# Kernel tuning notes

Measured on AMD Instinct MI355X. Metric: run time of the kernel, lower is better.

## Reference

```python
import jax, jax.numpy as jnp
import numpy as np

B, H, S, D, R = 2, 32, 1024, 128, 16
NB = 4  # max blocks: pre-image, image, pre-assistant-end, post-assistant


def _make_block_mask():
    # Synthetic but realistic block boundaries per sample (derived from the
    # image-token run and assistant-token subsequence positions that the torch
    # module extracts host-side from input_ids).
    bounds = [
        [(0, 16), (16, 272), (272, 603), (603, S)],
        [(0, 8), (8, 264), (264, 501), (501, S)],
    ]
    m = np.zeros((B, NB, S), np.float32)
    for b, blocks in enumerate(bounds):
        for n, (s, e) in enumerate(blocks):
            m[b, n, s:e] = 1.0
    return jnp.asarray(m)


def setup_inputs() -> dict:
    key = jax.random.key(0)
    ks = jax.random.split(key, 7)
    hid = H * D  # 4096
    lo = H * R   # 512
    causal_masked = ~jnp.tril(jnp.ones((S, S), bool))  # True = masked
    return {
        "query_states": jax.random.normal(ks[0], (B, H, S, D), jnp.float32),
        "key_states": jax.random.normal(ks[1], (B, H, S, D), jnp.float32),
        "Wqa": jax.random.normal(ks[2], (lo, hid), jnp.float32) / np.sqrt(hid),
        "Wqb": jax.random.normal(ks[3], (hid, lo), jnp.float32) / np.sqrt(lo),
        "Wka": jax.random.normal(ks[4], (lo, hid), jnp.float32) / np.sqrt(hid),
        "Wkb": jax.random.normal(ks[5], (hid, lo), jnp.float32) / np.sqrt(lo),
        "alpha": jax.random.normal(ks[6], (1,), jnp.float32) * 0.01,  # alpha_std
        "block_mask": _make_block_mask(),  # [B, NB, K] 1.0 inside block
        "attention_mask": jnp.broadcast_to(causal_masked, (B, 1, S, S)),
    }


def reference(query_states, key_states, Wqa, Wqb, Wka, Wkb, alpha, block_mask, attention_mask):
    Bb, Hh, Q, Dd = query_states.shape
    scaling = Dd ** -0.5

    # low-rank Q projection: [B,H,Q,D] -> [B,Q,H*D] -> rank -> back
    q = query_states.transpose(0, 2, 1, 3).reshape(Bb, Q, Hh * Dd)
    q = (q @ Wqa.T) @ Wqb.T
    q = q.reshape(Bb, Q, Hh, Dd).transpose(0, 2, 1, 3)

    Kk = key_states.shape[2]
    k = key_states.transpose(0, 2, 1, 3).reshape(Bb, Kk, Hh * Dd)
    k = (k @ Wka.T) @ Wkb.T
    k = k.reshape(Bb, Kk, Hh, Dd).transpose(0, 2, 1, 3)

    scores = jnp.einsum('bhqd,bhkd->bhqk', q, k) * scaling  # [B,H,Q,K]
    neg = jnp.finfo(scores.dtype).min
    scores = jnp.where(attention_mask, neg, scores)
    attn = jax.nn.softmax(scores, axis=-1)

    # block-wise mean pooling with causal-valid counts (mean_pool path)
    valid = (~attention_mask[:, 0]).astype(attn.dtype)       # [B,Q,K]
    masked_attn = attn * valid[:, None]                      # zero masked keys
    counts = jnp.einsum('bqk,bnk->bqn', valid, block_mask)   # [B,Q,NB]
    sums = jnp.einsum('bhqk,bnk->bhqn', masked_attn, block_mask)
    block_scores = sums / jnp.maximum(counts, 1.0)[:, None]  # [B,H,Q,NB]

    # expand block scores back to full [B,H,Q,K] and zero masked positions
    reweight = jnp.einsum('bhqn,bnk->bhqk', block_scores, block_mask)
    reweight = reweight * valid[:, None]
    return alpha[0] * reweight
```

## Files before the change

### kernel.cpp

```cpp
#include <hip/hip_runtime.h>
#include <hip/hip_bf16.h>

typedef float    f32x4 __attribute__((ext_vector_type(4)));
typedef _Float16 f16x8 __attribute__((ext_vector_type(8)));
typedef unsigned int u32;

#define S_LEN 1024
#define NHEAD 32
#define DHEAD 128
#define HID   4096
#define LORA  512
#define MROWS 2048

__device__ __forceinline__ void gload16(const void* g, const void* l) {
  __builtin_amdgcn_global_load_lds(
      (const __attribute__((address_space(1))) u32*)g,
      (__attribute__((address_space(3))) u32*)l, 16, 0, 0);
}

__device__ __forceinline__ f16x8 cvt8(f32x4 a, f32x4 b) {
  f16x8 r;
  r[0] = (_Float16)a[0]; r[1] = (_Float16)a[1];
  r[2] = (_Float16)a[2]; r[3] = (_Float16)a[3];
  r[4] = (_Float16)b[0]; r[5] = (_Float16)b[1];
  r[6] = (_Float16)b[2]; r[7] = (_Float16)b[3];
  return r;
}

__global__ __launch_bounds__(256) void gemm1_kernel(
    const float* __restrict__ Xq, const float* __restrict__ Wqa_,
    const float* __restrict__ Xk, const float* __restrict__ Wka_,
    float* __restrict__ Up)
{
  const int side = blockIdx.z >> 2, ks = blockIdx.z & 3;
  const float* X = side ? Xk : Xq;
  const float* W = side ? Wka_ : Wqa_;
  float* U = Up + ((size_t)(side * 4 + ks)) * (MROWS * LORA);

  __shared__ _Float16 As[2][128 * 32];
  __shared__ _Float16 Bs[2][128 * 32];

  const int t = threadIdx.x, lane = t & 63, w = t >> 6;
  const int wr = w >> 1, wc = w & 1;
  const int m0 = blockIdx.x * 128, n0 = blockIdx.y * 128;
  const int kbeg = ks * 1024;

  const int ar = t >> 1, ac = (t & 1) * 16;
  const int am = m0 + ar, ab = am >> 10, as_ = am & 1023;
  const float* Abase = X + (size_t)ab * (NHEAD * S_LEN * DHEAD) + (size_t)as_ * DHEAD;
  const float* Brow = W + (size_t)(n0 + ar) * HID;

  f16x8 ha0, ha1, hb0, hb1;
  auto LOADREGS = [&](int kt) {
    const int kg = kt + ac;
    const float* pa = Abase + (size_t)(kg >> 7) * (S_LEN * DHEAD) + (kg & 127);
    f32x4 a0 = *(const f32x4*)(pa + 0), a1 = *(const f32x4*)(pa + 4);
    f32x4 a2 = *(const f32x4*)(pa + 8), a3 = *(const f32x4*)(pa + 12);
    const float* pb = Brow + kg;
    f32x4 b0 = *(const f32x4*)(pb + 0), b1 = *(const f32x4*)(pb + 4);
    f32x4 b2 = *(const f32x4*)(pb + 8), b3 = *(const f32x4*)(pb + 12);
    ha0 = cvt8(a0, a1); ha1 = cvt8(a2, a3);
    hb0 = cvt8(b0, b1); hb1 = cvt8(b2, b3);
  };

  LOADREGS(kbeg);
  f32x4 acc[4][4] = {};

  for (int step = 0; step < 32; ++step) {
    const int cur = step & 1;
    *(f16x8*)&As[cur][ar * 32 + ac]     = ha0;
    *(f16x8*)&As[cur][ar * 32 + ac + 8] = ha1;
    *(f16x8*)&Bs[cur][ar * 32 + ac]     = hb0;
    *(f16x8*)&Bs[cur][ar * 32 + ac + 8] = hb1;
    __syncthreads();
    if (step + 1 < 32) LOADREGS(kbeg + (step + 1) * 32);
    f16x8 af[4], bf[4];
#pragma unroll
    for (int im = 0; im < 4; ++im)
      af[im] = *(const f16x8*)&As[cur][(wr * 64 + im * 16 + (lane & 15)) * 32 + (lane >> 4) * 8];
#pragma unroll
    for (int in = 0; in < 4; ++in)
      bf[in] = *(const f16x8*)&Bs[cur][(wc * 64 + in * 16 + (lane & 15)) * 32 + (lane >> 4) * 8];
#pragma unroll
    for (int im = 0; im < 4; ++im)
#pragma unroll
      for (int in = 0; in < 4; ++in)
        acc[im][in] = __builtin_amdgcn_mfma_f32_16x16x32_f16(af[im], bf[in], acc[im][in], 0, 0, 0);
  }

#pragma unroll
  for (int im = 0; im < 4; ++im)
#pragma unroll
    for (int in = 0; in < 4; ++in)
#pragma unroll
      for (int j = 0; j < 4; ++j) {
        const int m = m0 + wr * 64 + im * 16 + (lane >> 4) * 4 + j;
        const int n = n0 + wc * 64 + in * 16 + (lane & 15);
        U[(size_t)m * LORA + n] = acc[im][in][j];
      }
}

__global__ __launch_bounds__(256) void reduce_u(
    const float* __restrict__ Up, _Float16* __restrict__ Uq, _Float16* __restrict__ Uk)
{
  const int idx = blockIdx.x * 256 + threadIdx.x;
  const int side = idx >> 17;
  const int cc = idx & 131071;
  const float* base = Up + (size_t)side * 4 * (MROWS * LORA) + (size_t)cc * 8;
  f32x4 s0 = {0.f,0.f,0.f,0.f}, s1 = {0.f,0.f,0.f,0.f};
#pragma unroll
  for (int p = 0; p < 4; ++p) {
    const float* pp = base + (size_t)p * (MROWS * LORA);
    s0 += *(const f32x4*)(pp);
    s1 += *(const f32x4*)(pp + 4);
  }
  f16x8 h;
#pragma unroll
  for (int i = 0; i < 4; ++i) { h[i] = (_Float16)s0[i]; h[i + 4] = (_Float16)s1[i]; }
  _Float16* U = side ? Uk : Uq;
  *(f16x8*)(U + (size_t)cc * 8) = h;
}

__global__ __launch_bounds__(256) void gemm2_kernel(
    const _Float16* __restrict__ Uq, const float* __restrict__ Wqb_,
    const _Float16* __restrict__ Uk, const float* __restrict__ Wkb_,
    _Float16* __restrict__ Pq, _Float16* __restrict__ Pk)
{
  const _Float16* A = blockIdx.z ? Uk : Uq;
  const float*   Wf = blockIdx.z ? Wkb_ : Wqb_;
  _Float16*       P = blockIdx.z ? Pk : Pq;

  __shared__ _Float16 As[2][128 * 32];
  __shared__ _Float16 Bs[2][128 * 32];

  const int t = threadIdx.x, lane = t & 63, w = t >> 6;
  const int wr = w >> 1, wc = w & 1;
  const int m0 = blockIdx.x * 128, n0 = blockIdx.y * 128;

  const int o0 = w * 1024 + lane * 16;
  const int o1 = o0 + 4096;
  const int r0 = o0 >> 6, k0e = (o0 & 63) >> 1;
  const int r1 = o1 >> 6, k1e = (o1 & 63) >> 1;

  const int ar = t >> 1, ac = (t & 1) * 16;
  const float* Brow = Wf + (size_t)(n0 + ar) * LORA;

  auto GLOADA = [&](int buf, int kt) {
    char* AsB = (char*)As[buf];
    gload16(A + (size_t)(m0 + r0) * LORA + kt + k0e, AsB + w * 1024);
    gload16(A + (size_t)(m0 + r1) * LORA + kt + k1e, AsB + 4096 + w * 1024);
  };
  f16x8 hb0, hb1;
  auto LOADB = [&](int kt) {
    const float* pb = Brow + kt + ac;
    f32x4 b0 = *(const f32x4*)(pb + 0), b1 = *(const f32x4*)(pb + 4);
    f32x4 b2 = *(const f32x4*)(pb + 8), b3 = *(const f32x4*)(pb + 12);
    hb0 = cvt8(b0, b1); hb1 = cvt8(b2, b3);
  };

  LOADB(0);
  GLOADA(0, 0);
  f32x4 acc[4][4] = {};

  for (int step = 0; step < 16; ++step) {
    const int cur = step & 1;
    *(f16x8*)&Bs[cur][ar * 32 + ac]     = hb0;
    *(f16x8*)&Bs[cur][ar * 32 + ac + 8] = hb1;
    __syncthreads();
    if (step + 1 < 16) { LOADB((step + 1) * 32); GLOADA(cur ^ 1, (step + 1) * 32); }
    f16x8 af[4], bf[4];
#pragma unroll
    for (int im = 0; im < 4; ++im)
      af[im] = *(const f16x8*)&As[cur][(wr * 64 + im * 16 + (lane & 15)) * 32 + (lane >> 4) * 8];
#pragma unroll
    for (int in = 0; in < 4; ++in)
      bf[in] = *(const f16x8*)&Bs[cur][(wc * 64 + in * 16 + (lane & 15)) * 32 + (lane >> 4) * 8];
#pragma unroll
    for (int im = 0; im < 4; ++im)
#pragma unroll
      for (int in = 0; in < 4; ++in)
        acc[im][in] = __builtin_amdgcn_mfma_f32_16x16x32_f16(af[im], bf[in], acc[im][in], 0, 0, 0);
  }

#pragma unroll
  for (int im = 0; im < 4; ++im)
#pragma unroll
    for (int in = 0; in < 4; ++in)
#pragma unroll
      for (int j = 0; j < 4; ++j) {
        const int m = m0 + wr * 64 + im * 16 + (lane >> 4) * 4 + j;
        const int n = n0 + wc * 64 + in * 16 + (lane & 15);
        P[(size_t)m * HID + n] = (_Float16)acc[im][in][j];
      }
}

__global__ __launch_bounds__(256) void attn_kernel(
    const _Float16* __restrict__ QP, const _Float16* __restrict__ KP,
    const float* __restrict__ bmask, const float* __restrict__ alphap,
    float* __restrict__ out)
{
  __shared__ float    bm[1024 * 4];
  __shared__ _Float16 kv[2][64 * 136];
  __shared__ float    pfq[64 * 4];
  __shared__ float    bs_l[64 * 4];

  const int t = threadIdx.x;
  const int lane = t & 63, w = t >> 6;
  const int bh = blockIdx.x, b = bh >> 5, h = bh & 31;
  const int qb = (int)(gridDim.y - 1) - (int)blockIdx.y;

  for (int idx = t; idx < 4096; idx += 256) {
    const int nb = idx >> 10, k = idx & 1023;
    bm[k * 4 + nb] = bmask[(size_t)b * 4096 + idx];
  }
  __syncthreads();

  {
    float carry = 0.f;
    for (int seg = 0; seg <= qb; ++seg) {
      float v = bm[(seg * 64 + lane) * 4 + w];
#pragma unroll
      for (int d = 1; d < 64; d <<= 1) {
        float u = __shfl_up(v, d, 64);
        if (lane >= d) v += u;
      }
      if (seg == qb) pfq[lane * 4 + w] = v + carry;
      carry += __shfl(v, 63, 64);
    }
  }

  const int qrow = qb * 64 + w * 16 + (lane & 15);
  const _Float16* qrp = QP + (size_t)(b * 1024 + qrow) * HID + h * DHEAD;
  f16x8 a[4];
#pragma unroll
  for (int i = 0; i < 4; ++i)
    a[i] = *(const f16x8*)(qrp + i * 32 + (lane >> 4) * 8);

  float bsum[4][4] = {};
  const float scale = 0.08838834764831845f;

  const int r = t >> 2, c = (t & 3) * 32;
  const _Float16* kbase = KP + (size_t)(b * 1024) * HID + h * DHEAD;

  f16x8 k0, k1, k2, k3;
  auto LOADK = [&](int kt) {
    const _Float16* pk = kbase + (size_t)(kt * 64 + r) * HID + c;
    k0 = *(const f16x8*)(pk + 0);
    k1 = *(const f16x8*)(pk + 8);
    k2 = *(const f16x8*)(pk + 16);
    k3 = *(const f16x8*)(pk + 24);
  };
  LOADK(0);

  for (int kt = 0; kt <= qb; ++kt) {
    const int cur = kt & 1;
    *(f16x8*)&kv[cur][r * 136 + c + 0]  = k0;
    *(f16x8*)&kv[cur][r * 136 + c + 8]  = k1;
    *(f16x8*)&kv[cur][r * 136 + c + 16] = k2;
    *(f16x8*)&kv[cur][r * 136 + c + 24] = k3;
    __syncthreads();
    if (kt < qb) LOADK(kt + 1);

    const bool last = (kt == qb);
#pragma unroll
    for (int nt = 0; nt < 4; ++nt) {
      if (last && nt > w) break;
      f32x4 sacc = {0.f, 0.f, 0.f, 0.f};
#pragma unroll
      for (int i = 0; i < 4; ++i) {
        f16x8 bf = *(const f16x8*)&kv[cur][(nt * 16 + (lane & 15)) * 136 + i * 32 + (lane >> 4) * 8];
        sacc = __builtin_amdgcn_mfma_f32_16x16x32_f16(a[i], bf, sacc, 0, 0, 0);
      }
      const int kk = kt * 64 + nt * 16 + (lane & 15);
      f32x4 mv = *(const f32x4*)&bm[kk * 4];
      const bool diag = last && (nt == w);
#pragma unroll
      for (int j = 0; j < 4; ++j) {
        float e = __expf(sacc[j] * scale);
        if (diag) {
          const int q = qb * 64 + w * 16 + (lane >> 4) * 4 + j;
          e = (kk <= q) ? e : 0.f;
        }
        bsum[0][j] += e * mv[0];
        bsum[1][j] += e * mv[1];
        bsum[2][j] += e * mv[2];
        bsum[3][j] += e * mv[3];
      }
    }
  }

#pragma unroll
  for (int j = 0; j < 4; ++j)
#pragma unroll
    for (int m = 1; m < 16; m <<= 1)
#pragma unroll
      for (int nb = 0; nb < 4; ++nb)
        bsum[nb][j] += __shfl_xor(bsum[nb][j], m, 64);

  const float alpha = alphap[0];
  if ((lane & 15) == 0) {
#pragma unroll
    for (int j = 0; j < 4; ++j) {
      const int rr = w * 16 + (lane >> 4) * 4 + j;
      const float Lr = bsum[0][j] + bsum[1][j] + bsum[2][j] + bsum[3][j];
      const float ainvL = alpha / Lr;
#pragma unroll
      for (int nb = 0; nb < 4; ++nb)
        bs_l[rr * 4 + nb] = bsum[nb][j] * ainvL / fmaxf(pfq[rr * 4 + nb], 1.f);
    }
  }
  __syncthreads();

  const size_t obase = ((size_t)bh * 1024 + (size_t)qb * 64) * 1024;
  const int k0i = t * 4;
  f32x4 m0v = *(const f32x4*)&bm[(k0i + 0) * 4];
  f32x4 m1v = *(const f32x4*)&bm[(k0i + 1) * 4];
  f32x4 m2v = *(const f32x4*)&bm[(k0i + 2) * 4];
  f32x4 m3v = *(const f32x4*)&bm[(k0i + 3) * 4];
  for (int rr = 0; rr < 64; ++rr) {
    const int q = qb * 64 + rr;
    f32x4 bsv = *(const f32x4*)&bs_l[rr * 4];
    f32x4 o;
    o[0] = (k0i + 0 <= q) ? (bsv[0]*m0v[0] + bsv[1]*m0v[1] + bsv[2]*m0v[2] + bsv[3]*m0v[3]) : 0.f;
    o[1] = (k0i + 1 <= q) ? (bsv[0]*m1v[0] + bsv[1]*m1v[1] + bsv[2]*m1v[2] + bsv[3]*m1v[3]) : 0.f;
    o[2] = (k0i + 2 <= q) ? (bsv[0]*m2v[0] + bsv[1]*m2v[1] + bsv[2]*m2v[2] + bsv[3]*m2v[3]) : 0.f;
    o[3] = (k0i + 3 <= q) ? (bsv[0]*m3v[0] + bsv[1]*m3v[1] + bsv[2]*m3v[2] + bsv[3]*m3v[3]) : 0.f;
    *(f32x4*)(out + obase + (size_t)rr * 1024 + k0i) = o;
  }
}

extern "C" void kernel_launch(void* const* d_in, const int* in_sizes, int n_in,
                              void* d_out, int out_size, void* d_ws, size_t ws_size,
                              hipStream_t stream) {
  const float* q     = (const float*)d_in[0];
  const float* k     = (const float*)d_in[1];
  const float* Wqa   = (const float*)d_in[2];
  const float* Wqb   = (const float*)d_in[3];
  const float* Wka   = (const float*)d_in[4];
  const float* Wkb   = (const float*)d_in[5];
  const float* alpha = (const float*)d_in[6];
  const float* bmask = (const float*)d_in[7];
  float* out = (float*)d_out;

  _Float16* Uq = (_Float16*)d_ws;
  _Float16* Uk = Uq + (size_t)MROWS * LORA;
  _Float16* Pq = Uk + (size_t)MROWS * LORA;
  _Float16* Pk = Pq + (size_t)MROWS * HID;
  float*    Up = (float*)(Pk + (size_t)MROWS * HID);

  gemm1_kernel<<<dim3(16, 4, 8), 256, 0, stream>>>(q, Wqa, k, Wka, Up);
  reduce_u    <<<1024, 256, 0, stream>>>(Up, Uq, Uk);
  gemm2_kernel<<<dim3(16, 32, 2), 256, 0, stream>>>(Uq, Wqb, Uk, Wkb, Pq, Pk);
  attn_kernel <<<dim3(64, 16), 256, 0, stream>>>(Pq, Pk, bmask, alpha, out);
}
```

Baseline: 466.6 us.

## Pre-convert weights to fp16 and stream them into LDS via direct global loads

Adds a kernel that converts all four projection weight matrices from fp32 to fp16 once per call. The two GEMMs then load the weight tiles with global_load_lds straight into shared memory instead of loading fp32 into registers, converting and storing. This halves weight read traffic inside the GEMMs and drops register staging, at the cost of an extra launch and an extra pass over the weights. The block mask in the attention kernel is also kept as fp16 in LDS to reduce shared memory use.

```diff
diff --git a/kernel.cpp b/kernel.cpp
--- a/kernel.cpp
+++ b/kernel.cpp
@@ -3,6 +3,7 @@
 
 typedef float    f32x4 __attribute__((ext_vector_type(4)));
 typedef _Float16 f16x8 __attribute__((ext_vector_type(8)));
+typedef _Float16 f16x4 __attribute__((ext_vector_type(4)));
 typedef unsigned int u32;
 
 #define S_LEN 1024
@@ -27,14 +28,34 @@
   return r;
 }
 
+#define WCH 262144
+
+__global__ __launch_bounds__(256) void convertW_kernel(
+    const float* __restrict__ Wqa, const float* __restrict__ Wka,
+    const float* __restrict__ Wqb, const float* __restrict__ Wkb,
+    _Float16* __restrict__ WaqH, _Float16* __restrict__ WakH,
+    _Float16* __restrict__ WbqH, _Float16* __restrict__ WbkH)
+{
+  const float* Ws[4] = {Wqa, Wka, Wqb, Wkb};
+  _Float16*    Wd[4] = {WaqH, WakH, WbqH, WbkH};
+  for (int c = blockIdx.x * 256 + threadIdx.x; c < 4 * WCH; c += 1024 * 256) {
+    const int seg = c >> 18;
+    const int off = (c & (WCH - 1)) * 8;
+    const float* src = Ws[seg] + off;
+    f32x4 v0 = *(const f32x4*)(src + 0);
+    f32x4 v1 = *(const f32x4*)(src + 4);
+    *(f16x8*)(Wd[seg] + off) = cvt8(v0, v1);
+  }
+}
+
 __global__ __launch_bounds__(256) void gemm1_kernel(
-    const float* __restrict__ Xq, const float* __restrict__ Wqa_,
-    const float* __restrict__ Xk, const float* __restrict__ Wka_,
+    const float* __restrict__ Xq, const _Float16* __restrict__ WaqH,
+    const float* __restrict__ Xk, const _Float16* __restrict__ WakH,
     float* __restrict__ Up)
 {
   const int side = blockIdx.z >> 2, ks = blockIdx.z & 3;
   const float* X = side ? Xk : Xq;
-  const float* W = side ? Wka_ : Wqa_;
+  const _Float16* WH = side ? WakH : WaqH;
   float* U = Up + ((size_t)(side * 4 + ks)) * (MROWS * LORA);
 
   __shared__ _Float16 As[2][128 * 32];
@@ -48,32 +69,36 @@
   const int ar = t >> 1, ac = (t & 1) * 16;
   const int am = m0 + ar, ab = am >> 10, as_ = am & 1023;
   const float* Abase = X + (size_t)ab * (NHEAD * S_LEN * DHEAD) + (size_t)as_ * DHEAD;
-  const float* Brow = W + (size_t)(n0 + ar) * HID;
-
-  f16x8 ha0, ha1, hb0, hb1;
-  auto LOADREGS = [&](int kt) {
+
+  const int o0 = w * 1024 + lane * 16;
+  const int o1 = o0 + 4096;
+  const int r0 = o0 >> 6, k0e = (o0 & 63) >> 1;
+  const int r1 = o1 >> 6, k1e = (o1 & 63) >> 1;
+
+  auto GLOADB = [&](int buf, int kt) {
+    char* BsB = (char*)Bs[buf];
+    gload16(WH + (size_t)(n0 + r0) * HID + kt + k0e, BsB + w * 1024);
+    gload16(WH + (size_t)(n0 + r1) * HID + kt + k1e, BsB + 4096 + w * 1024);
+  };
+  f16x8 ha0, ha1;
+  auto LOADA = [&](int kt) {
     const int kg = kt + ac;
     const float* pa = Abase + (size_t)(kg >> 7) * (S_LEN * DHEAD) + (kg & 127);
     f32x4 a0 = *(const f32x4*)(pa + 0), a1 = *(const f32x4*)(pa + 4);
     f32x4 a2 = *(const f32x4*)(pa + 8), a3 = *(const f32x4*)(pa + 12);
-    const float* pb = Brow + kg;
-    f32x4 b0 = *(const f32x4*)(pb + 0), b1 = *(const f32x4*)(pb + 4);
-    f32x4 b2 = *(const f32x4*)(pb + 8), b3 = *(const f32x4*)(pb + 12);
     ha0 = cvt8(a0, a1); ha1 = cvt8(a2, a3);
-    hb0 = cvt8(b0, b1); hb1 = cvt8(b2, b3);
   };
 
-  LOADREGS(kbeg);
+  GLOADB(0, kbeg);
+  LOADA(kbeg);
   f32x4 acc[4][4] = {};
 
   for (int step = 0; step < 32; ++step) {
     const int cur = step & 1;
     *(f16x8*)&As[cur][ar * 32 + ac]     = ha0;
     *(f16x8*)&As[cur][ar * 32 + ac + 8] = ha1;
-    *(f16x8*)&Bs[cur][ar * 32 + ac]     = hb0;
-    *(f16x8*)&Bs[cur][ar * 32 + ac + 8] = hb1;
     __syncthreads();
-    if (step + 1 < 32) LOADREGS(kbeg + (step + 1) * 32);
+    if (step + 1 < 32) { GLOADB(cur ^ 1, kbeg + (step + 1) * 32); LOADA(kbeg + (step + 1) * 32); }
     f16x8 af[4], bf[4];
 #pragma unroll
     for (int im = 0; im < 4; ++im)
@@ -122,12 +147,12 @@
 }
 
 __global__ __launch_bounds__(256) void gemm2_kernel(
-    const _Float16* __restrict__ Uq, const float* __restrict__ Wqb_,
-    const _Float16* __restrict__ Uk, const float* __restrict__ Wkb_,
+    const _Float16* __restrict__ Uq, const _Float16* __restrict__ WbqH,
+    const _Float16* __restrict__ Uk, const _Float16* __restrict__ WbkH,
     _Float16* __restrict__ Pq, _Float16* __restrict__ Pk)
 {
   const _Float16* A = blockIdx.z ? Uk : Uq;
-  const float*   Wf = blockIdx.z ? Wkb_ : Wqb_;
+  const _Float16* B = blockIdx.z ? WbkH : WbqH;
   _Float16*       P = blockIdx.z ? Pk : Pq;
 
   __shared__ _Float16 As[2][128 * 32];
@@ -142,32 +167,22 @@
   const int r0 = o0 >> 6, k0e = (o0 & 63) >> 1;
   const int r1 = o1 >> 6, k1e = (o1 & 63) >> 1;
 
-  const int ar = t >> 1, ac = (t & 1) * 16;
-  const float* Brow = Wf + (size_t)(n0 + ar) * LORA;
-
-  auto GLOADA = [&](int buf, int kt) {
+  auto GLOADAB = [&](int buf, int kt) {
     char* AsB = (char*)As[buf];
+    char* BsB = (char*)Bs[buf];
     gload16(A + (size_t)(m0 + r0) * LORA + kt + k0e, AsB + w * 1024);
     gload16(A + (size_t)(m0 + r1) * LORA + kt + k1e, AsB + 4096 + w * 1024);
+    gload16(B + (size_t)(n0 + r0) * LORA + kt + k0e, BsB + w * 1024);
+    gload16(B + (size_t)(n0 + r1) * LORA + kt + k1e, BsB + 4096 + w * 1024);
   };
-  f16x8 hb0, hb1;
-  auto LOADB = [&](int kt) {
-    const float* pb = Brow + kt + ac;
-    f32x4 b0 = *(const f32x4*)(pb + 0), b1 = *(const f32x4*)(pb + 4);
-    f32x4 b2 = *(const f32x4*)(pb + 8), b3 = *(const f32x4*)(pb + 12);
-    hb0 = cvt8(b0, b1); hb1 = cvt8(b2, b3);
-  };
-
-  LOADB(0);
-  GLOADA(0, 0);
+
+  GLOADAB(0, 0);
   f32x4 acc[4][4] = {};
 
   for (int step = 0; step < 16; ++step) {
     const int cur = step & 1;
-    *(f16x8*)&Bs[cur][ar * 32 + ac]     = hb0;
-    *(f16x8*)&Bs[cur][ar * 32 + ac + 8] = hb1;
     __syncthreads();
-    if (step + 1 < 16) { LOADB((step + 1) * 32); GLOADA(cur ^ 1, (step + 1) * 32); }
+    if (step + 1 < 16) GLOADAB(cur ^ 1, (step + 1) * 32);
     f16x8 af[4], bf[4];
 #pragma unroll
     for (int im = 0; im < 4; ++im)
@@ -199,7 +214,7 @@
     const float* __restrict__ bmask, const float* __restrict__ alphap,
     float* __restrict__ out)
 {
-  __shared__ float    bm[1024 * 4];
+  __shared__ _Float16 bm_h[1024 * 4];
   __shared__ _Float16 kv[2][64 * 136];
   __shared__ float    pfq[64 * 4];
   __shared__ float    bs_l[64 * 4];
@@ -211,14 +226,14 @@
 
   for (int idx = t; idx < 4096; idx += 256) {
     const int nb = idx >> 10, k = idx & 1023;
-    bm[k * 4 + nb] = bmask[(size_t)b * 4096 + idx];
+    bm_h[k * 4 + nb] = (_Float16)bmask[(size_t)b * 4096 + idx];
   }
   __syncthreads();
 
   {
     float carry = 0.f;
     for (int seg = 0; seg <= qb; ++seg) {
-      float v = bm[(seg * 64 + lane) * 4 + w];
+      float v = (float)bm_h[(seg * 64 + lane) * 4 + w];
 #pragma unroll
       for (int d = 1; d < 64; d <<= 1) {
         float u = __shfl_up(v, d, 64);
@@ -272,7 +287,9 @@
         sacc = __builtin_amdgcn_mfma_f32_16x16x32_f16(a[i], bf, sacc, 0, 0, 0);
       }
       const int kk = kt * 64 + nt * 16 + (lane & 15);
-      f32x4 mv = *(const f32x4*)&bm[kk * 4];
+      const f16x4 mh = *(const f16x4*)&bm_h[kk * 4];
+      const float mv0 = (float)mh[0], mv1 = (float)mh[1];
+      const float mv2 = (float)mh[2], mv3 = (float)mh[3];
       const bool diag = last && (nt == w);
 #pragma unroll
       for (int j = 0; j < 4; ++j) {
@@ -281,10 +298,10 @@
           const int q = qb * 64 + w * 16 + (lane >> 4) * 4 + j;
           e = (kk <= q) ? e : 0.f;
         }
-        bsum[0][j] += e * mv[0];
-        bsum[1][j] += e * mv[1];
-        bsum[2][j] += e * mv[2];
-        bsum[3][j] += e * mv[3];
+        bsum[0][j] += e * mv0;
+        bsum[1][j] += e * mv1;
+        bsum[2][j] += e * mv2;
+        bsum[3][j] += e * mv3;
       }
     }
   }
@@ -313,18 +330,21 @@
 
   const size_t obase = ((size_t)bh * 1024 + (size_t)qb * 64) * 1024;
   const int k0i = t * 4;
-  f32x4 m0v = *(const f32x4*)&bm[(k0i + 0) * 4];
-  f32x4 m1v = *(const f32x4*)&bm[(k0i + 1) * 4];
-  f32x4 m2v = *(const f32x4*)&bm[(k0i + 2) * 4];
-  f32x4 m3v = *(const f32x4*)&bm[(k0i + 3) * 4];
+  f32x4 mv[4];
+#pragma unroll
+  for (int i = 0; i < 4; ++i) {
+    const f16x4 mh = *(const f16x4*)&bm_h[(k0i + i) * 4];
+    mv[i][0] = (float)mh[0]; mv[i][1] = (float)mh[1];
+    mv[i][2] = (float)mh[2]; mv[i][3] = (float)mh[3];
+  }
   for (int rr = 0; rr < 64; ++rr) {
     const int q = qb * 64 + rr;
     f32x4 bsv = *(const f32x4*)&bs_l[rr * 4];
     f32x4 o;
-    o[0] = (k0i + 0 <= q) ? (bsv[0]*m0v[0] + bsv[1]*m0v[1] + bsv[2]*m0v[2] + bsv[3]*m0v[3]) : 0.f;
-    o[1] = (k0i + 1 <= q) ? (bsv[0]*m1v[0] + bsv[1]*m1v[1] + bsv[2]*m1v[2] + bsv[3]*m1v[3]) : 0.f;
-    o[2] = (k0i + 2 <= q) ? (bsv[0]*m2v[0] + bsv[1]*m2v[1] + bsv[2]*m2v[2] + bsv[3]*m2v[3]) : 0.f;
-    o[3] = (k0i + 3 <= q) ? (bsv[0]*m3v[0] + bsv[1]*m3v[1] + bsv[2]*m3v[2] + bsv[3]*m3v[3]) : 0.f;
+#pragma unroll
+    for (int i = 0; i < 4; ++i)
+      o[i] = (k0i + i <= q)
+           ? (bsv[0]*mv[i][0] + bsv[1]*mv[i][1] + bsv[2]*mv[i][2] + bsv[3]*mv[i][3]) : 0.f;
     *(f32x4*)(out + obase + (size_t)rr * 1024 + k0i) = o;
   }
 }
@@ -342,14 +362,19 @@
   const float* bmask = (const float*)d_in[7];
   float* out = (float*)d_out;
 
-  _Float16* Uq = (_Float16*)d_ws;
-  _Float16* Uk = Uq + (size_t)MROWS * LORA;
-  _Float16* Pq = Uk + (size_t)MROWS * LORA;
-  _Float16* Pk = Pq + (size_t)MROWS * HID;
-  float*    Up = (float*)(Pk + (size_t)MROWS * HID);
-
-  gemm1_kernel<<<dim3(16, 4, 8), 256, 0, stream>>>(q, Wqa, k, Wka, Up);
+  _Float16* WaqH = (_Float16*)d_ws;
+  _Float16* WakH = WaqH + (size_t)LORA * HID;
+  _Float16* WbqH = WakH + (size_t)LORA * HID;
+  _Float16* WbkH = WbqH + (size_t)HID * LORA;
+  _Float16* Uq   = WbkH + (size_t)HID * LORA;
+  _Float16* Uk   = Uq   + (size_t)MROWS * LORA;
+  _Float16* Pq   = Uk   + (size_t)MROWS * LORA;
+  _Float16* Pk   = Pq   + (size_t)MROWS * HID;
+  float*    Up   = (float*)(Pk + (size_t)MROWS * HID);
+
+  convertW_kernel<<<1024, 256, 0, stream>>>(Wqa, Wka, Wqb, Wkb, WaqH, WakH, WbqH, WbkH);
+  gemm1_kernel<<<dim3(16, 4, 8), 256, 0, stream>>>(q, WaqH, k, WakH, Up);
   reduce_u    <<<1024, 256, 0, stream>>>(Up, Uq, Uk);
-  gemm2_kernel<<<dim3(16, 32, 2), 256, 0, stream>>>(Uq, Wqb, Uk, Wkb, Pq, Pk);
+  gemm2_kernel<<<dim3(16, 32, 2), 256, 0, stream>>>(Uq, WbqH, Uk, WbkH, Pq, Pk);
   attn_kernel <<<dim3(64, 16), 256, 0, stream>>>(Pq, Pk, bmask, alpha, out);
 }
```

Result: faster. 450.0 us (-3.6%).
